# Kernel tuning notes

Hardware: AMD Instinct MI355X
Metric: run time of the kernel (lower is better)

## Reference

```python
import jax, jax.numpy as jnp
import numpy as np

T, B, D, H, A = 512, 256, 512, 256, 32

def setup_inputs() -> dict:
    key = jax.random.key(0)
    ks = jax.random.split(key, 8)
    s_in = 1.0 / np.sqrt(D)
    s_h = 1.0 / np.sqrt(H)
    return {
        "inputs": jax.random.normal(ks[0], (T, B, D), dtype=jnp.float32),
        "is_new_episode": jax.random.randint(ks[1], (T, B, 1), 0, 2, dtype=jnp.int32),
        "carry_c": jax.random.normal(ks[2], (B, H), dtype=jnp.float32),
        "carry_h": jax.random.normal(ks[3], (B, H), dtype=jnp.float32),
        "Wx": jax.random.normal(ks[4], (D, 4 * H), dtype=jnp.float32) * s_in,
        "Wh": jax.random.normal(ks[5], (H, 4 * H), dtype=jnp.float32) * s_h,
        "b": jnp.zeros((4 * H,), dtype=jnp.float32),
        "Wa": jax.random.normal(ks[6], (H, A), dtype=jnp.float32) * s_h,
        "ba": jnp.zeros((A,), dtype=jnp.float32),
        "Wv": jax.random.normal(ks[7], (H, 1), dtype=jnp.float32) * s_h,
        "bv": jnp.zeros((1,), dtype=jnp.float32),
    }

def reference(inputs, is_new_episode, carry_c, carry_h, Wx, Wh, b, Wa, ba, Wv, bv):
    # Precompute the input projection for all timesteps in one big GEMM:
    # [T,B,D] @ [D,4H] -> [T,B,4H]
    x_proj = jnp.einsum('tbd,dk->tbk', inputs, Wx) + b

    def step(carry, xs):
        c, h = carry
        xp, new_ep = xs  # xp: [B,4H], new_ep: [B,1] int
        reset = new_ep.reshape(-1, 1) != 0  # 'zero' new-episode handling
        c = jnp.where(reset, 0.0, c)
        h = jnp.where(reset, 0.0, h)
        z = xp + h @ Wh  # [B,4H]
        i, f, g, o = jnp.split(z, 4, axis=-1)
        new_c = jax.nn.sigmoid(f) * c + jax.nn.sigmoid(i) * jnp.tanh(g)
        new_h = jax.nn.sigmoid(o) * jnp.tanh(new_c)
        mu = new_h @ Wa + ba            # [B,A]
        value = new_h @ Wv + bv         # [B,1]
        out = jnp.concatenate([mu, value], axis=-1)  # [B,A+1]
        return (new_c, new_h), out

    (c_fin, h_fin), outs = jax.lax.scan(step, (carry_c, carry_h),
                                        (x_proj, is_new_episode))
    return outs  # [T,B,A+1]: per-step (mu, value)
```

## Files before the change

kernel.cpp:

```cpp
#include <hip/hip_runtime.h>
#include <hip/hip_bf16.h>
#include <stdint.h>

#define TT 512
#define BB 256
#define DD 512
#define HH 256
#define AA 32
#define NG 1024

using f32x4 = __attribute__((ext_vector_type(4))) float;
using bf8   = __attribute__((ext_vector_type(8))) short;

static __device__ __forceinline__ short f2bf(float f) {
  union { float f; uint32_t u; } v; v.f = f;
  uint32_t u = v.u;
  u = u + 0x7fffu + ((u >> 16) & 1u);
  return (short)(u >> 16);
}
static __device__ __forceinline__ float bf2f(unsigned short s) {
  union { uint32_t u; float f; } v; v.u = ((uint32_t)s) << 16;
  return v.f;
}
static __device__ __forceinline__ float sigf(float x) {
  return 1.0f / (1.0f + __expf(-x));
}
static __device__ __forceinline__ float tanh_(float x) {
  float e = __expf(2.0f * x);
  return 1.0f - 2.0f / (e + 1.0f);
}

static constexpr size_t XP_OFF    = 0;
static constexpr size_t XP_BYTES  = (size_t)TT * BB * NG * 2;
static constexpr size_t WXT_OFF   = XP_OFF + XP_BYTES;
static constexpr size_t WXT_BYTES = (size_t)NG * DD * 2;
static constexpr size_t MAIL_OFF  = WXT_OFF + WXT_BYTES;
static constexpr size_t MAIL_BYTES= (size_t)2 * 16 * 2 * 16 * 128 * 4;
static constexpr size_t DONE_OFF   = MAIL_OFF + MAIL_BYTES;
static constexpr size_t DONE_BYTES = (size_t)TT * 16 * 4;
static constexpr size_t WS_NEEDED      = MAIL_OFF + MAIL_BYTES;
static constexpr size_t WS_NEEDED_FUSE = DONE_OFF + DONE_BYTES;

__global__ __launch_bounds__(256) void transpose_wx_kernel(
    const float* __restrict__ Wx, unsigned short* __restrict__ WxT) {
  __shared__ float tile[32][33];
  int bx = blockIdx.x;
  int k0 = (bx & 15) * 32;
  int n0 = (bx >> 4) * 32;
  int r = threadIdx.x >> 5;
  int c = threadIdx.x & 31;
  #pragma unroll
  for (int i = 0; i < 4; ++i) {
    int rr = r + i * 8;
    tile[rr][c] = Wx[(size_t)(k0 + rr) * NG + n0 + c];
  }
  __syncthreads();
  #pragma unroll
  for (int i = 0; i < 4; ++i) {
    int rr = r + i * 8;
    WxT[(size_t)(n0 + rr) * DD + k0 + c] = (unsigned short)f2bf(tile[c][rr]);
  }
}

__global__ __launch_bounds__(256) void gemm_xproj(
    const float* __restrict__ X,
    const unsigned short* __restrict__ WxT,
    const float* __restrict__ bias,
    unsigned short* __restrict__ xp) {
  __shared__ short As[128][72];
  __shared__ short Bs[128][72];
  const int tid  = threadIdx.x;
  const int lane = tid & 63;
  const int wave = tid >> 6;
  const int quad = lane >> 4;
  const int l15  = lane & 15;
  const int wm = wave >> 1, wn = wave & 1;
  const int bid = blockIdx.x;
  const int m0 = (bid >> 3) * 128;
  const int n0 = (bid & 7) * 128;

  f32x4 acc[4][4];
  #pragma unroll
  for (int i = 0; i < 4; ++i)
    #pragma unroll
    for (int j = 0; j < 4; ++j) acc[i][j] = (f32x4){0.f, 0.f, 0.f, 0.f};

  for (int kt = 0; kt < 8; ++kt) {
    const int k0 = kt * 64;
    #pragma unroll
    for (int jj = 0; jj < 4; ++jj) {
      int c = tid + jj * 256;
      int row = c >> 3;
      int kc = (c & 7) * 8;
      const float4* src = (const float4*)(X + (size_t)(m0 + row) * DD + k0 + kc);
      float4 v0 = src[0];
      float4 v1 = src[1];
      bf8 tv;
      tv[0] = f2bf(v0.x); tv[1] = f2bf(v0.y); tv[2] = f2bf(v0.z); tv[3] = f2bf(v0.w);
      tv[4] = f2bf(v1.x); tv[5] = f2bf(v1.y); tv[6] = f2bf(v1.z); tv[7] = f2bf(v1.w);
      *(bf8*)&As[row][kc] = tv;
      const uint4* bsrc = (const uint4*)(WxT + (size_t)(n0 + row) * DD + k0 + kc);
      *(uint4*)&Bs[row][kc] = *bsrc;
    }
    __syncthreads();
    #pragma unroll
    for (int ks = 0; ks < 2; ++ks) {
      bf8 a[4], b[4];
      #pragma unroll
      for (int mt = 0; mt < 4; ++mt)
        a[mt] = *(const bf8*)&As[wm * 64 + mt * 16 + l15][ks * 32 + quad * 8];
      #pragma unroll
      for (int nt = 0; nt < 4; ++nt)
        b[nt] = *(const bf8*)&Bs[wn * 64 + nt * 16 + l15][ks * 32 + quad * 8];
      #pragma unroll
      for (int mt = 0; mt < 4; ++mt)
        #pragma unroll
        for (int nt = 0; nt < 4; ++nt)
          acc[mt][nt] = __builtin_amdgcn_mfma_f32_16x16x32_bf16(a[mt], b[nt], acc[mt][nt], 0, 0, 0);
    }
    __syncthreads();
  }
  #pragma unroll
  for (int mt = 0; mt < 4; ++mt)
    #pragma unroll
    for (int nt = 0; nt < 4; ++nt) {
      int col = n0 + wn * 64 + nt * 16 + l15;
      float bv = bias[col];
      #pragma unroll
      for (int r = 0; r < 4; ++r) {
        int row = m0 + wm * 64 + mt * 16 + quad * 4 + r;
        xp[(size_t)row * NG + col] = (unsigned short)f2bf(acc[mt][nt][r] + bv);
      }
    }
}

template <bool FUSED>
static __device__ __forceinline__ void scan_body(
    char* smem,
    const unsigned short* __restrict__ xp,
    const int* __restrict__ is_new,
    const float* __restrict__ carry_c,
    const float* __restrict__ carry_h,
    const float* __restrict__ Wh,
    const float* __restrict__ Wa,
    const float* __restrict__ ba,
    const float* __restrict__ Wv,
    const float* __restrict__ bv,
    float* __restrict__ out,
    unsigned int* __restrict__ mail,
    unsigned int* __restrict__ done) {
  const int tid  = threadIdx.x;
  const int lane = tid & 63;
  const int w    = tid >> 6;
  const int quad = (lane >> 4);
  const int l15  = lane & 15;
  const int bid  = blockIdx.x;
  const int grp  = bid >> 1;
  const int p    = bid & 1;
  const int s    = p * 8 + w;
  const int b0   = grp * 16;
  const int j0   = s * 16;

  short (*h_lds)[264]  = (short (*)[264])smem;
  int   (*flag_lds)[16] = (int (*)[16])(smem + 8448);

  bf8 whb[4][8];
  #pragma unroll
  for (int nt = 0; nt < 4; ++nt)
    #pragma unroll
    for (int ks = 0; ks < 8; ++ks)
      #pragma unroll
      for (int j = 0; j < 8; ++j) {
        int k = ks * 32 + quad * 8 + j;
        int col = nt * 256 + j0 + l15;
        whb[nt][ks][j] = f2bf(Wh[(size_t)k * NG + col]);
      }
  const int astart = (s < 15) ? (2 * s) : 30;
  const int ncols  = (s < 15) ? 2 : 3;
  bf8 wab[8];
  #pragma unroll
  for (int ks = 0; ks < 8; ++ks)
    #pragma unroll
    for (int j = 0; j < 8; ++j) {
      int k = ks * 32 + quad * 8 + j;
      float v = 0.0f;
      if (l15 < ncols) {
        int a = astart + l15;
        v = (a < 32) ? Wa[(size_t)k * 32 + a] : Wv[k];
      }
      wab[ks][j] = f2bf(v);
    }
  float obias = 0.0f;
  if (l15 < ncols) {
    int a = astart + l15;
    obias = (a < 32) ? ba[a] : bv[0];
  }
  float c4[4];
  #pragma unroll
  for (int r = 0; r < 4; ++r)
    c4[r] = carry_c[(size_t)(b0 + quad * 4 + r) * HH + j0 + l15];

  const int crow = tid >> 5;
  const int cc0  = (tid & 31) * 4;

  bool rdy = false;

  #pragma unroll 1
  for (int t = 0; t <= TT; ++t) {
    const bool last = (t == TT);
    unsigned short xpraw[16];
    unsigned int dv = 0u;
    if (!last) {
      if constexpr (FUSED) {
        if (!rdy) {
          const unsigned int want = 0x5EED0000u | (unsigned)t;
          unsigned int* dp = done + (size_t)t * 16 + l15;
          int g2 = 0;
          for (;;) {
            unsigned int v = __hip_atomic_load(dp, __ATOMIC_RELAXED, __HIP_MEMORY_SCOPE_AGENT);
            if (__all((int)(v == want))) break;
            __builtin_amdgcn_s_sleep(8);
            if (++g2 > (1 << 20)) break;
          }
        }
        __atomic_signal_fence(__ATOMIC_ACQUIRE);
      }
      #pragma unroll
      for (int nt = 0; nt < 4; ++nt)
        #pragma unroll
        for (int r = 0; r < 4; ++r) {
          size_t row = (size_t)t * BB + b0 + quad * 4 + r;
          xpraw[nt * 4 + r] = xp[row * NG + nt * 256 + j0 + l15];
        }
      if (tid < 16) flag_lds[t & 1][tid] = is_new[t * BB + b0 + tid];
      if constexpr (FUSED) {
        if (t + 1 < TT)
          dv = __hip_atomic_load(done + (size_t)(t + 1) * 16 + l15,
                                 __ATOMIC_RELAXED, __HIP_MEMORY_SCOPE_AGENT);
      }
    }
    if (t > 0) {
      unsigned long long* mp = (unsigned long long*)
          (mail + ((((size_t)(t & 1) * 16 + grp) * 2 + (1 - p)) * 2048)
                + (size_t)crow * 128 + cc0);
      const unsigned long long M = 0xFFFF0000FFFF0000ull;
      const unsigned long long Wt = ((unsigned long long)(unsigned)t << 16)
                                  | ((unsigned long long)(unsigned)t << 48);
      unsigned long long pv0, pv1;
      int guard = 0;
      for (;;) {
        pv0 = __hip_atomic_load(&mp[0], __ATOMIC_RELAXED, __HIP_MEMORY_SCOPE_AGENT);
        pv1 = __hip_atomic_load(&mp[1], __ATOMIC_RELAXED, __HIP_MEMORY_SCOPE_AGENT);
        bool ok = ((pv0 & M) == Wt) && ((pv1 & M) == Wt);
        if (__all((int)ok)) break;
        __builtin_amdgcn_s_sleep(1);
        if (++guard > (1 << 24)) break;
      }
      __atomic_signal_fence(__ATOMIC_ACQUIRE);
      unsigned long long packed =
            (pv0 & 0xFFFFull)
          | (((pv0 >> 32) & 0xFFFFull) << 16)
          | ((pv1 & 0xFFFFull) << 32)
          | (((pv1 >> 32) & 0xFFFFull) << 48);
      *(unsigned long long*)&h_lds[crow][(1 - p) * 128 + cc0] = packed;
    } else {
      int row  = tid >> 5;
      int col0 = (tid & 31) * 8;
      const float4* src = (const float4*)(carry_h + (size_t)(b0 + row) * HH + col0);
      float4 a = src[0], b4 = src[1];
      bf8 tv;
      tv[0] = f2bf(a.x);  tv[1] = f2bf(a.y);  tv[2] = f2bf(a.z);  tv[3] = f2bf(a.w);
      tv[4] = f2bf(b4.x); tv[5] = f2bf(b4.y); tv[6] = f2bf(b4.z); tv[7] = f2bf(b4.w);
      *(bf8*)&h_lds[row][col0] = tv;
    }
    __syncthreads();
    bf8 af[8];
    #pragma unroll
    for (int ks = 0; ks < 8; ++ks)
      af[ks] = *(const bf8*)&h_lds[l15][ks * 32 + quad * 8];
    __syncthreads();
    if (!last) {
      f32x4 zacc[4];
      #pragma unroll
      for (int nt = 0; nt < 4; ++nt) zacc[nt] = (f32x4){0.f, 0.f, 0.f, 0.f};
      #pragma unroll
      for (int ks = 0; ks < 8; ++ks)
        #pragma unroll
        for (int nt = 0; nt < 4; ++nt)
          zacc[nt] = __builtin_amdgcn_mfma_f32_16x16x32_bf16(af[ks], whb[nt][ks], zacc[nt], 0, 0, 0);
      unsigned int* mout = mail + ((((size_t)((t + 1) & 1) * 16 + grp) * 2 + p) * 2048);
      const unsigned int tag = (unsigned int)(t + 1) << 16;
      #pragma unroll
      for (int r = 0; r < 4; ++r) {
        int fr = flag_lds[t & 1][quad * 4 + r];
        float zi = (fr ? 0.0f : zacc[0][r]) + bf2f(xpraw[0 * 4 + r]);
        float zf = (fr ? 0.0f : zacc[1][r]) + bf2f(xpraw[1 * 4 + r]);
        float zg = (fr ? 0.0f : zacc[2][r]) + bf2f(xpraw[2 * 4 + r]);
        float zo = (fr ? 0.0f : zacc[3][r]) + bf2f(xpraw[3 * 4 + r]);
        float ce = fr ? 0.0f : c4[r];
        float ncv = sigf(zf) * ce + sigf(zi) * tanh_(zg);
        c4[r] = ncv;
        float nh = sigf(zo) * tanh_(ncv);
        unsigned short hv = (unsigned short)f2bf(nh);
        int row = quad * 4 + r;
        h_lds[row][j0 + l15] = (short)hv;
        __hip_atomic_store(&mout[(size_t)row * 128 + w * 16 + l15],
                           (unsigned int)hv | tag,
                           __ATOMIC_RELAXED, __HIP_MEMORY_SCOPE_AGENT);
      }
    }
    if constexpr (FUSED) {
      rdy = (!last && (t + 1 < TT))
          ? (bool)__all((int)(dv == (0x5EED0000u | (unsigned)(t + 1))))
          : false;
    }
    if (t > 0) {
      f32x4 oacc = {0.f, 0.f, 0.f, 0.f};
      #pragma unroll
      for (int ks = 0; ks < 8; ++ks)
        oacc = __builtin_amdgcn_mfma_f32_16x16x32_bf16(af[ks], wab[ks], oacc, 0, 0, 0);
      if (l15 < ncols) {
        #pragma unroll
        for (int r = 0; r < 4; ++r) {
          size_t orow = (size_t)(t - 1) * BB + b0 + quad * 4 + r;
          out[orow * 33 + astart + l15] = oacc[r] + obias;
        }
      }
    }
  }
}

__global__ __launch_bounds__(512, 1) void scan_kernel(
    const unsigned short* __restrict__ xp,
    const int* __restrict__ is_new,
    const float* __restrict__ carry_c,
    const float* __restrict__ carry_h,
    const float* __restrict__ Wh,
    const float* __restrict__ Wa,
    const float* __restrict__ ba,
    const float* __restrict__ Wv,
    const float* __restrict__ bv,
    float* __restrict__ out,
    unsigned int* __restrict__ mail) {
  __shared__ __align__(16) char smem[8576];
  scan_body<false>(smem, xp, is_new, carry_c, carry_h, Wh, Wa, ba, Wv, bv,
                   out, mail, nullptr);
}

__global__ __launch_bounds__(512, 1) void fused_kernel(
    const float* __restrict__ X,
    const unsigned short* __restrict__ WxT,
    const float* __restrict__ bias,
    unsigned short* __restrict__ xp,
    const int* __restrict__ is_new,
    const float* __restrict__ carry_c,
    const float* __restrict__ carry_h,
    const float* __restrict__ Wh,
    const float* __restrict__ Wa,
    const float* __restrict__ ba,
    const float* __restrict__ Wv,
    const float* __restrict__ bv,
    float* __restrict__ out,
    unsigned int* __restrict__ mail,
    unsigned int* __restrict__ done) {
  __shared__ __align__(16) char smem[86016];
  const int tid = threadIdx.x;
  if (blockIdx.x >= 32) {
    short (*As)[72] = (short (*)[72])smem;
    short (*Bs)[72] = (short (*)[72])(smem + 18432);
    const int lane = tid & 63;
    const int wave = tid >> 6;
    const int quad = lane >> 4;
    const int l15  = lane & 15;
    const int wm = wave >> 1;
    const int wn = wave & 1;
    const int bid_g = (int)blockIdx.x - 32;
    const int mtile = bid_g >> 3;
    const int nb    = bid_g & 7;
    const int m0 = mtile * 128;
    const int n0 = nb * 128;

    f32x4 acc[2][4];
    #pragma unroll
    for (int i = 0; i < 2; ++i)
      #pragma unroll
      for (int j = 0; j < 4; ++j) acc[i][j] = (f32x4){0.f, 0.f, 0.f, 0.f};

    for (int kt = 0; kt < 8; ++kt) {
      const int k0 = kt * 64;
      #pragma unroll
      for (int jj = 0; jj < 2; ++jj) {
        int c = tid + jj * 512;
        int row = c >> 3;
        int kc = (c & 7) * 8;
        const float4* src = (const float4*)(X + (size_t)(m0 + row) * DD + k0 + kc);
        float4 v0 = src[0];
        float4 v1 = src[1];
        bf8 tv;
        tv[0] = f2bf(v0.x); tv[1] = f2bf(v0.y); tv[2] = f2bf(v0.z); tv[3] = f2bf(v0.w);
        tv[4] = f2bf(v1.x); tv[5] = f2bf(v1.y); tv[6] = f2bf(v1.z); tv[7] = f2bf(v1.w);
        *(bf8*)&As[row][kc] = tv;
        const uint4* bsrc = (const uint4*)(WxT + (size_t)(n0 + row) * DD + k0 + kc);
        *(uint4*)&Bs[row][kc] = *bsrc;
      }
      __syncthreads();
      #pragma unroll
      for (int ks = 0; ks < 2; ++ks) {
        bf8 a[2], b[4];
        #pragma unroll
        for (int mt = 0; mt < 2; ++mt)
          a[mt] = *(const bf8*)&As[wm * 32 + mt * 16 + l15][ks * 32 + quad * 8];
        #pragma unroll
        for (int nt = 0; nt < 4; ++nt)
          b[nt] = *(const bf8*)&Bs[wn * 64 + nt * 16 + l15][ks * 32 + quad * 8];
        #pragma unroll
        for (int mt = 0; mt < 2; ++mt)
          #pragma unroll
          for (int nt = 0; nt < 4; ++nt)
            acc[mt][nt] = __builtin_amdgcn_mfma_f32_16x16x32_bf16(a[mt], b[nt], acc[mt][nt], 0, 0, 0);
      }
      __syncthreads();
    }
    #pragma unroll
    for (int mt = 0; mt < 2; ++mt)
      #pragma unroll
      for (int nt = 0; nt < 4; ++nt) {
        int col = n0 + wn * 64 + nt * 16 + l15;
        float bvv = bias[col];
        #pragma unroll
        for (int r = 0; r < 4; ++r) {
          int row = m0 + wm * 32 + mt * 16 + quad * 4 + r;
          xp[(size_t)row * NG + col] = (unsigned short)f2bf(acc[mt][nt][r] + bvv);
        }
      }
    __syncthreads();
    if (tid == 0) {
      __builtin_amdgcn_fence(__ATOMIC_RELEASE, "agent");
      const int t16  = mtile >> 1;
      const int slot = (mtile & 1) * 8 + nb;
      __hip_atomic_store(&done[(size_t)t16 * 16 + slot],
                         0x5EED0000u | (unsigned)t16,
                         __ATOMIC_RELAXED, __HIP_MEMORY_SCOPE_AGENT);
    }
    return;
  }
  scan_body<true>(smem, xp, is_new, carry_c, carry_h, Wh, Wa, ba, Wv, bv,
                  out, mail, done);
}

extern "C" void kernel_launch(void* const* d_in, const int* in_sizes, int n_in,
                              void* d_out, int out_size, void* d_ws, size_t ws_size,
                              hipStream_t stream) {
  const float* X       = (const float*)d_in[0];
  const int* is_new    = (const int*)d_in[1];
  const float* carry_c = (const float*)d_in[2];
  const float* carry_h = (const float*)d_in[3];
  const float* Wx      = (const float*)d_in[4];
  const float* Wh      = (const float*)d_in[5];
  const float* b       = (const float*)d_in[6];
  const float* Wa      = (const float*)d_in[7];
  const float* ba      = (const float*)d_in[8];
  const float* Wv      = (const float*)d_in[9];
  const float* bv      = (const float*)d_in[10];
  float* out = (float*)d_out;
  char* ws = (char*)d_ws;
  if (ws_size < WS_NEEDED) return;
  unsigned short* xp   = (unsigned short*)(ws + XP_OFF);
  unsigned short* WxT  = (unsigned short*)(ws + WXT_OFF);
  unsigned int* mail   = (unsigned int*)(ws + MAIL_OFF);

  hipLaunchKernelGGL(transpose_wx_kernel, dim3(512), dim3(256), 0, stream, Wx, WxT);
  if (ws_size >= WS_NEEDED_FUSE) {
    unsigned int* done = (unsigned int*)(ws + DONE_OFF);
    hipLaunchKernelGGL(fused_kernel, dim3(32 + 8192), dim3(512), 0, stream,
                       X, WxT, b, xp, is_new, carry_c, carry_h, Wh, Wa, ba, Wv, bv,
                       out, mail, done);
  } else {
    hipLaunchKernelGGL(gemm_xproj, dim3(8192), dim3(256), 0, stream, X, WxT, b, xp);
    hipLaunchKernelGGL(scan_kernel, dim3(32), dim3(512), 0, stream,
                       xp, is_new, carry_c, carry_h, Wh, Wa, ba, Wv, bv, out, mail);
  }
}
```

Before: 2.467 ms.

## Use persistent throttled producer blocks for input projection in fused LSTM kernel

```diff
diff --git a/kernel.cpp b/kernel.cpp
--- a/kernel.cpp
+++ b/kernel.cpp
@@ -8,6 +8,9 @@
 #define HH 256
 #define AA 32
 #define NG 1024
+
+#define NPROD 192
+#define THROTTLE_K 24
 
 using f32x4 = __attribute__((ext_vector_type(4))) float;
 using bf8   = __attribute__((ext_vector_type(8))) short;
@@ -38,8 +41,10 @@
 static constexpr size_t MAIL_BYTES= (size_t)2 * 16 * 2 * 16 * 128 * 4;
 static constexpr size_t DONE_OFF   = MAIL_OFF + MAIL_BYTES;
 static constexpr size_t DONE_BYTES = (size_t)TT * 16 * 4;
+static constexpr size_t PROG_OFF   = DONE_OFF + DONE_BYTES;
+static constexpr size_t PROG_BYTES = 256;
 static constexpr size_t WS_NEEDED      = MAIL_OFF + MAIL_BYTES;
-static constexpr size_t WS_NEEDED_FUSE = DONE_OFF + DONE_BYTES;
+static constexpr size_t WS_NEEDED_FUSE = PROG_OFF + PROG_BYTES;
 
 __global__ __launch_bounds__(256) void transpose_wx_kernel(
     const float* __restrict__ Wx, unsigned short* __restrict__ WxT) {
@@ -148,7 +153,8 @@
     const float* __restrict__ bv,
     float* __restrict__ out,
     unsigned int* __restrict__ mail,
-    unsigned int* __restrict__ done) {
+    unsigned int* __restrict__ done,
+    unsigned int* __restrict__ prog) {
   const int tid  = threadIdx.x;
   const int lane = tid & 63;
   const int w    = tid >> 6;
@@ -212,6 +218,9 @@
     unsigned int dv = 0u;
     if (!last) {
       if constexpr (FUSED) {
+        if (p == 0 && tid == 0)
+          __hip_atomic_store(&prog[grp], 0x5EED0000u | (unsigned)t,
+                             __ATOMIC_RELAXED, __HIP_MEMORY_SCOPE_AGENT);
         if (!rdy) {
           const unsigned int want = 0x5EED0000u | (unsigned)t;
           unsigned int* dp = done + (size_t)t * 16 + l15;
@@ -230,7 +239,16 @@
         #pragma unroll
         for (int r = 0; r < 4; ++r) {
           size_t row = (size_t)t * BB + b0 + quad * 4 + r;
-          xpraw[nt * 4 + r] = xp[row * NG + nt * 256 + j0 + l15];
+          if constexpr (FUSED) {
+            size_t col = (size_t)nt * 256 + j0 + (l15 & ~1);
+            unsigned int v = __hip_atomic_load(
+                (unsigned int*)(xp + row * NG + col),
+                __ATOMIC_RELAXED, __HIP_MEMORY_SCOPE_AGENT);
+            xpraw[nt * 4 + r] =
+                (unsigned short)((l15 & 1) ? (v >> 16) : (v & 0xFFFFu));
+          } else {
+            xpraw[nt * 4 + r] = xp[row * NG + nt * 256 + j0 + l15];
+          }
         }
       if (tid < 16) flag_lds[t & 1][tid] = is_new[t * BB + b0 + tid];
       if constexpr (FUSED) {
@@ -344,7 +362,7 @@
     unsigned int* __restrict__ mail) {
   __shared__ __align__(16) char smem[8576];
   scan_body<false>(smem, xp, is_new, carry_c, carry_h, Wh, Wa, ba, Wv, bv,
-                   out, mail, nullptr);
+                   out, mail, nullptr, nullptr);
 }
 
 __global__ __launch_bounds__(512, 1) void fused_kernel(
@@ -362,90 +380,121 @@
     const float* __restrict__ bv,
     float* __restrict__ out,
     unsigned int* __restrict__ mail,
-    unsigned int* __restrict__ done) {
+    unsigned int* __restrict__ done,
+    unsigned int* __restrict__ prog) {
   __shared__ __align__(16) char smem[86016];
   const int tid = threadIdx.x;
   if (blockIdx.x >= 32) {
     short (*As)[72] = (short (*)[72])smem;
     short (*Bs)[72] = (short (*)[72])(smem + 18432);
+    short* xps = (short*)smem;
     const int lane = tid & 63;
     const int wave = tid >> 6;
     const int quad = lane >> 4;
     const int l15  = lane & 15;
     const int wm = wave >> 1;
     const int wn = wave & 1;
-    const int bid_g = (int)blockIdx.x - 32;
-    const int mtile = bid_g >> 3;
-    const int nb    = bid_g & 7;
-    const int m0 = mtile * 128;
-    const int n0 = nb * 128;
-
-    f32x4 acc[2][4];
-    #pragma unroll
-    for (int i = 0; i < 2; ++i)
-      #pragma unroll
-      for (int j = 0; j < 4; ++j) acc[i][j] = (f32x4){0.f, 0.f, 0.f, 0.f};
-
-    for (int kt = 0; kt < 8; ++kt) {
-      const int k0 = kt * 64;
-      #pragma unroll
-      for (int jj = 0; jj < 2; ++jj) {
-        int c = tid + jj * 512;
-        int row = c >> 3;
-        int kc = (c & 7) * 8;
-        const float4* src = (const float4*)(X + (size_t)(m0 + row) * DD + k0 + kc);
-        float4 v0 = src[0];
-        float4 v1 = src[1];
-        bf8 tv;
-        tv[0] = f2bf(v0.x); tv[1] = f2bf(v0.y); tv[2] = f2bf(v0.z); tv[3] = f2bf(v0.w);
-        tv[4] = f2bf(v1.x); tv[5] = f2bf(v1.y); tv[6] = f2bf(v1.z); tv[7] = f2bf(v1.w);
-        *(bf8*)&As[row][kc] = tv;
-        const uint4* bsrc = (const uint4*)(WxT + (size_t)(n0 + row) * DD + k0 + kc);
-        *(uint4*)&Bs[row][kc] = *bsrc;
+    const int pid = (int)blockIdx.x - 32;
+
+    for (int tile = pid; tile < 8192; tile += NPROD) {
+      const int mtile = tile >> 3;
+      const int nb    = tile & 7;
+      const int t16   = mtile >> 1;
+      const int m0 = mtile * 128;
+      const int n0 = nb * 128;
+
+      if (tid == 0) {
+        int g = 0;
+        for (;;) {
+          int mn = 0x7FFFFFFF;
+          #pragma unroll
+          for (int i = 0; i < 16; ++i) {
+            unsigned int pv = __hip_atomic_load(&prog[i], __ATOMIC_RELAXED,
+                                                __HIP_MEMORY_SCOPE_AGENT);
+            int pt = ((pv >> 16) == 0x5EEDu) ? (int)(pv & 0xFFFFu) : 0;
+            mn = pt < mn ? pt : mn;
+          }
+          if (t16 < mn + THROTTLE_K) break;
+          __builtin_amdgcn_s_sleep(16);
+          if (++g > (1 << 12)) break;
+        }
       }
       __syncthreads();
-      #pragma unroll
-      for (int ks = 0; ks < 2; ++ks) {
-        bf8 a[2], b[4];
-        #pragma unroll
-        for (int mt = 0; mt < 2; ++mt)
-          a[mt] = *(const bf8*)&As[wm * 32 + mt * 16 + l15][ks * 32 + quad * 8];
-        #pragma unroll
-        for (int nt = 0; nt < 4; ++nt)
-          b[nt] = *(const bf8*)&Bs[wn * 64 + nt * 16 + l15][ks * 32 + quad * 8];
-        #pragma unroll
-        for (int mt = 0; mt < 2; ++mt)
+
+      f32x4 acc[2][4];
+      #pragma unroll
+      for (int i = 0; i < 2; ++i)
+        #pragma unroll
+        for (int j = 0; j < 4; ++j) acc[i][j] = (f32x4){0.f, 0.f, 0.f, 0.f};
+
+      for (int kt = 0; kt < 8; ++kt) {
+        const int k0 = kt * 64;
+        #pragma unroll
+        for (int jj = 0; jj < 2; ++jj) {
+          int c = tid + jj * 512;
+          int row = c >> 3;
+          int kc = (c & 7) * 8;
+          const float4* src = (const float4*)(X + (size_t)(m0 + row) * DD + k0 + kc);
+          float4 v0 = src[0];
+          float4 v1 = src[1];
+          bf8 tv;
+          tv[0] = f2bf(v0.x); tv[1] = f2bf(v0.y); tv[2] = f2bf(v0.z); tv[3] = f2bf(v0.w);
+          tv[4] = f2bf(v1.x); tv[5] = f2bf(v1.y); tv[6] = f2bf(v1.z); tv[7] = f2bf(v1.w);
+          *(bf8*)&As[row][kc] = tv;
+          const uint4* bsrc = (const uint4*)(WxT + (size_t)(n0 + row) * DD + k0 + kc);
+          *(uint4*)&Bs[row][kc] = *bsrc;
+        }
+        __syncthreads();
+        #pragma unroll
+        for (int ks = 0; ks < 2; ++ks) {
+          bf8 a[2], b[4];
+          #pragma unroll
+          for (int mt = 0; mt < 2; ++mt)
+            a[mt] = *(const bf8*)&As[wm * 32 + mt * 16 + l15][ks * 32 + quad * 8];
           #pragma unroll
           for (int nt = 0; nt < 4; ++nt)
-            acc[mt][nt] = __builtin_amdgcn_mfma_f32_16x16x32_bf16(a[mt], b[nt], acc[mt][nt], 0, 0, 0);
-      }
+            b[nt] = *(const bf8*)&Bs[wn * 64 + nt * 16 + l15][ks * 32 + quad * 8];
+          #pragma unroll
+          for (int mt = 0; mt < 2; ++mt)
+            #pragma unroll
+            for (int nt = 0; nt < 4; ++nt)
+              acc[mt][nt] = __builtin_amdgcn_mfma_f32_16x16x32_bf16(a[mt], b[nt], acc[mt][nt], 0, 0, 0);
+        }
+        __syncthreads();
+      }
+      #pragma unroll
+      for (int mt = 0; mt < 2; ++mt)
+        #pragma unroll
+        for (int nt = 0; nt < 4; ++nt) {
+          int lcol = wn * 64 + nt * 16 + l15;
+          float bvv = bias[n0 + lcol];
+          #pragma unroll
+          for (int r = 0; r < 4; ++r) {
+            int lrow = wm * 32 + mt * 16 + quad * 4 + r;
+            xps[lrow * 136 + lcol] = f2bf(acc[mt][nt][r] + bvv);
+          }
+        }
       __syncthreads();
-    }
-    #pragma unroll
-    for (int mt = 0; mt < 2; ++mt)
-      #pragma unroll
-      for (int nt = 0; nt < 4; ++nt) {
-        int col = n0 + wn * 64 + nt * 16 + l15;
-        float bvv = bias[col];
-        #pragma unroll
-        for (int r = 0; r < 4; ++r) {
-          int row = m0 + wm * 32 + mt * 16 + quad * 4 + r;
-          xp[(size_t)row * NG + col] = (unsigned short)f2bf(acc[mt][nt][r] + bvv);
-        }
-      }
-    __syncthreads();
-    if (tid == 0) {
-      __builtin_amdgcn_fence(__ATOMIC_RELEASE, "agent");
-      const int t16  = mtile >> 1;
-      const int slot = (mtile & 1) * 8 + nb;
-      __hip_atomic_store(&done[(size_t)t16 * 16 + slot],
-                         0x5EED0000u | (unsigned)t16,
-                         __ATOMIC_RELAXED, __HIP_MEMORY_SCOPE_AGENT);
+      #pragma unroll
+      for (int j = 0; j < 4; ++j) {
+        int c = tid + j * 512;
+        int row = c >> 4;
+        int seg = c & 15;
+        uint4 v = *(const uint4*)&xps[row * 136 + seg * 8];
+        *(uint4*)(xp + (size_t)(m0 + row) * NG + n0 + seg * 8) = v;
+      }
+      __syncthreads();
+      if (tid == 0) {
+        const int slot = (mtile & 1) * 8 + nb;
+        __hip_atomic_store(&done[(size_t)t16 * 16 + slot],
+                           0x5EED0000u | (unsigned)t16,
+                           __ATOMIC_RELEASE, __HIP_MEMORY_SCOPE_AGENT);
+      }
     }
     return;
   }
   scan_body<true>(smem, xp, is_new, carry_c, carry_h, Wh, Wa, ba, Wv, bv,
-                  out, mail, done);
+                  out, mail, done, prog);
 }
 
 extern "C" void kernel_launch(void* const* d_in, const int* in_sizes, int n_in,
@@ -472,9 +521,10 @@
   hipLaunchKernelGGL(transpose_wx_kernel, dim3(512), dim3(256), 0, stream, Wx, WxT);
   if (ws_size >= WS_NEEDED_FUSE) {
     unsigned int* done = (unsigned int*)(ws + DONE_OFF);
-    hipLaunchKernelGGL(fused_kernel, dim3(32 + 8192), dim3(512), 0, stream,
+    unsigned int* prog = (unsigned int*)(ws + PROG_OFF);
+    hipLaunchKernelGGL(fused_kernel, dim3(32 + NPROD), dim3(512), 0, stream,
                        X, WxT, b, xp, is_new, carry_c, carry_h, Wh, Wa, ba, Wv, bv,
-                       out, mail, done);
+                       out, mail, done, prog);
   } else {
     hipLaunchKernelGGL(gemm_xproj, dim3(8192), dim3(256), 0, stream, X, WxT, b, xp);
     hipLaunchKernelGGL(scan_kernel, dim3(32), dim3(512), 0, stream,
```

Measured after the change: 3.280 ms. 32.9% more time.
